# Performance work log

Measured on AMD Instinct MI355X. Metric: run time of the kernel, lower is better.

## Reference

```python
import jax, jax.numpy as jnp
import numpy as np

B, N = 32, 1000
HID, COM = 256, 64
T_LEN, NOP = 288, 3
NVAL, TP_D, CS_D, TIME_D = 9, 2, 4, 4
IN_C = CS_D + TP_D + NVAL            # 15, competition GAT input
IN_CO = IN_C + COM                    # 79, cooperation GAT input
OBS = TIME_D + TP_D + CS_D + 2 * COM + NVAL  # 147
K_D = K_F = 500                       # int(0.5*N + 0.5)
TEMP = 1.0
NEG = jnp.float32(-1e8)


def setup_inputs() -> dict:
    key = jax.random.key(0)
    ks = jax.random.split(key, 24)
    def nrm(k, shp, scale=0.05):
        return (jax.random.normal(k, shp, dtype=jnp.float32) * scale)
    return {
        "time_idx": jax.random.randint(ks[0], (B, N), 0, T_LEN, dtype=jnp.int32),
        "op_idx": jax.random.randint(ks[1], (B, N), 0, NOP, dtype=jnp.int32),
        "value_feats": jax.random.normal(ks[2], (B, N, NVAL), dtype=jnp.float32),
        "dpcs_mark": jax.random.randint(ks[3], (B, N, 1), 0, 2) > 0,
        "adj_comp": jax.random.randint(ks[4], (B, N, N), 0, 2) > 0,
        "adj_coop": jax.random.randint(ks[5], (B, N, N), 0, 2) > 0,
        "distance": jax.random.uniform(ks[6], (N, N), dtype=jnp.float32),
        "time_tab": jax.random.uniform(ks[7], (T_LEN, TIME_D), dtype=jnp.float32),
        "tp_tab": jax.random.uniform(ks[8], (NOP, TP_D), dtype=jnp.float32),
        "cs_tab": jax.random.uniform(ks[9], (N, CS_D), dtype=jnp.float32),
        "Wc": nrm(ks[10], (IN_C, COM)),
        "asrc_c": nrm(ks[11], (COM,)),
        "adst_c": nrm(ks[12], (COM,)),
        "wd_c": jnp.float32(0.1),
        "Wco": nrm(ks[13], (IN_CO, COM)),
        "asrc_co": nrm(ks[14], (COM,)),
        "adst_co": nrm(ks[15], (COM,)),
        "wd_co": jnp.float32(0.1),
        "Wp": nrm(ks[16], (OBS, HID)),
        "bp": jnp.zeros((HID,), dtype=jnp.float32),
        "vpd": nrm(ks[17], (HID,)),
        "vpf": nrm(ks[18], (HID,)),
    }


def gat(x, W, a_src, a_dst, w_d, adj, dist):
    """Single-head GAT over dense boolean adjacency. adj[b,j,i] True => edge j->i."""
    h = jnp.einsum("bnf,fd->bnd", x, W)                       # (B,N,D)
    e = (jnp.einsum("bid,d->bi", h, a_dst)[:, :, None]        # dst term
         + jnp.einsum("bjd,d->bj", h, a_src)[:, None, :]      # src term
         + w_d * dist.T[None])                                 # dist[j,i] edge feat
    e = jax.nn.leaky_relu(e, 0.2)
    mask = jnp.swapaxes(adj, 1, 2)                             # (B, dst i, src j)
    e = jnp.where(mask, e, NEG)
    alpha = jax.nn.softmax(e, axis=-1)
    alpha = jnp.where(mask, alpha, 0.0)                        # isolated nodes -> 0
    return jax.nn.elu(jnp.einsum("bij,bjd->bid", alpha, h))


def gated_pool(x_p, scores, valid, k, temp):
    scores = scores - scores.max(axis=1, keepdims=True)
    scores = jnp.where(valid, scores, NEG)                     # (B,N,1)
    val_topk = jax.lax.top_k(scores[..., 0], k)[0]             # (B,k)
    min_topk = val_topk.min(axis=-1)[:, None, None]
    scores = jnp.where(scores < min_topk, NEG, scores)
    w = jax.nn.softmax(scores / temp, axis=1)
    xg = x_p * w
    return jnp.concatenate([xg.sum(axis=1), xg.max(axis=1)], axis=-1)  # (B,2H)


def reference(time_idx, op_idx, value_feats, dpcs_mark, adj_comp, adj_coop,
              distance, time_tab, tp_tab, cs_tab, Wc, asrc_c, adst_c, wd_c,
              Wco, asrc_co, adst_co, wd_co, Wp, bp, vpd, vpf):
    time_e = time_tab[time_idx]                                # (B,N,4)
    tp_e = tp_tab[op_idx]                                      # (B,N,2)
    cs_e = jnp.broadcast_to(cs_tab[None], (B, N, CS_D))        # (B,N,4)
    vf_det = jax.lax.stop_gradient(value_feats)
    x = jnp.concatenate([cs_e, tp_e, vf_det], axis=-1)         # (B,N,15)
    comp_reps = gat(x, Wc, asrc_c, adst_c, wd_c, adj_comp, distance)
    x_m = jnp.concatenate([x, comp_reps], axis=-1)             # (B,N,79)
    coop_reps = gat(x_m, Wco, asrc_co, adst_co, wd_co, adj_coop, distance)
    sag = jnp.concatenate([time_e, cs_e, tp_e, value_feats, comp_reps, coop_reps], axis=-1)
    x_p = jnp.einsum("bnf,fh->bnh", sag, Wp) + bp              # (B,N,HID)
    scores_d = jnp.einsum("bnh,h->bn", x_p, vpd)[..., None]
    s_d = gated_pool(x_p, scores_d, dpcs_mark, K_D, TEMP)
    scores_f = jnp.einsum("bnh,h->bn", x_p, vpf)[..., None]
    s_f = gated_pool(x_p, scores_f, ~dpcs_mark, K_F, TEMP)
    return jnp.concatenate([s_f, s_d], axis=-1)                # (B, 4*HID)
```

## Files before the change

kernel.cpp:

```cpp
#include <hip/hip_runtime.h>
#include <hip/hip_bf16.h>

#define NB 32
#define NN 1000
#define COMD 64
#define HIDD 256
#define KSEL 500
#define TI 16
#define GATX ((NN + TI - 1) / TI)
#define PACKX 32
#define NSPL 32
#define ROWS 32
#define DSTRIDE 1024

#define PB_AQ1  0
#define PB_DT   1024
#define PB_WP   1280
#define PB_WCO  1320
#define PB_MISC 1344
#define PB_EMB  1345
#define PB_N    (PB_EMB + NB * NN / 4)

typedef __hip_bfloat16 bf16;
typedef unsigned long long u64;
typedef __attribute__((ext_vector_type(4))) float f32x4;
typedef __attribute__((ext_vector_type(8))) short s16x8;
typedef __attribute__((ext_vector_type(4))) short s16x4;
typedef __attribute__((ext_vector_type(4))) unsigned short u16x4;
typedef __attribute__((ext_vector_type(2))) unsigned long long u64x2;

__device__ __forceinline__ float b2f(bf16 x){ return __bfloat162float(x); }

template<bool F32>
__device__ __forceinline__ float ldf(const void* p, long i){
  return F32 ? ((const float*)p)[i] : b2f(((const bf16*)p)[i]);
}
__device__ __forceinline__ float ldr(const void* p, long i, int f32){
  return f32 ? ((const float*)p)[i] : b2f(((const bf16*)p)[i]);
}

__device__ __forceinline__ float wave_sum(float v){
#pragma unroll
  for (int o = 32; o > 0; o >>= 1) v += __shfl_down(v, o, 64);
  return v;
}
__device__ __forceinline__ float wave_bsum(float v){
#pragma unroll
  for (int o = 32; o > 0; o >>= 1) v += __shfl_xor(v, o, 64);
  return v;
}
__device__ __forceinline__ float wave_bmax(float v){
#pragma unroll
  for (int o = 32; o > 0; o >>= 1) v = fmaxf(v, __shfl_xor(v, o, 64));
  return v;
}
__device__ __forceinline__ int wave_bsum_i(int v){
#pragma unroll
  for (int o = 32; o > 0; o >>= 1) v += __shfl_xor(v, o, 64);
  return v;
}
__device__ __forceinline__ unsigned fkey(float f){
  unsigned u = __float_as_uint(f);
  return (u & 0x80000000u) ? ~u : (u | 0x80000000u);
}
__device__ __forceinline__ void split_bf(float v, short& hi, short& lo){
  unsigned u = __float_as_uint(v);
  float hf = __uint_as_float(u & 0xFFFF0000u);
  hi = (short)(u >> 16);
  float r = v - hf;
  lo = (short)(__float_as_uint(r) >> 16);
}
__device__ __forceinline__ short f2bs(float v){
  bf16 h = __float2bfloat16(v);
  short s; __builtin_memcpy(&s, &h, 2); return s;
}
__device__ __forceinline__ void hB_write(short* hB_hi, short* hB_lo,
                                         int b, int n, int ch, float v){
  int kb = n >> 5, g4 = (n >> 3) & 3, u = n & 7;
  long off = ((((long)b * 32 + kb) * 4 + g4) * 64 + ch) * 8 + u;
  short hi, lo; split_bf(v, hi, lo);
  hB_hi[off] = hi; hB_lo[off] = lo;
}
__device__ __forceinline__ void sniff2(const void* dist, const void* adjc,
                                       int lane, int& f32, int& as_int){
  unsigned wdist = ((const unsigned*)dist)[lane];
  unsigned wadj  = ((const unsigned*)adjc)[lane];
  f32 = (__ballot((wdist & 0xFFFFu) >= 0x8000u) != 0ull) ? 1 : 0;
  as_int = (__ballot(wadj > 1u) == 0ull) ? 1 : 0;
}

#define SMEM_BYTES 8704

template<bool F32>
__device__ __forceinline__ void dist_t_role(const void* dist, bf16* distTb,
                                            int rel, void* sm){
  bf16 (*tile)[68] = (bf16 (*)[68])sm;
  int t = threadIdx.x;
  int wv = t >> 6, lane = t & 63;
  int it = (rel & 15) * 64, jt = (rel >> 4) * 64;
#pragma unroll
  for (int r = 0; r < 16; ++r){
    int jl = r * 4 + wv;
    int j = jt + jl, i = it + lane;
    float v = (j < NN && i < NN) ? ldf<F32>(dist, (long)j * NN + i) : 0.f;
    tile[jl][lane] = __float2bfloat16(v);
  }
  __syncthreads();
#pragma unroll
  for (int r = 0; r < 16; ++r){
    int il = r * 4 + wv;
    int i = it + il, j = jt + lane;
    if (i < NN) distTb[(long)i * DSTRIDE + j] = tile[lane][il];
  }
}
template<bool BINT>
__device__ __forceinline__ void adjq_role(const void* adj, u64* adjQ,
                                          int rel, void* sm){
  u64 (*aw)[33] = (u64 (*)[33])sm;
  int t = threadIdx.x;
  int wv = t >> 6, lane = t & 63;
  int j0 = (rel & 31) * 32;
  int b  = rel >> 5;
  int ch3 = (192 + lane < 250) ? (192 + lane) : 249;
  int chk[4] = { lane, 64 + lane, 128 + lane, ch3 };
  long row0;
  {
    int j = j0 + wv * 8;
    int jc = (j < NN) ? j : (NN - 1);
    row0 = ((long)b * NN + jc) * (long)NN;
  }
  if (BINT){
    const int* base = (const int*)adj;
    uint4 cur[4], nxt[4];
#pragma unroll
    for (int c = 0; c < 4; ++c)
      cur[c] = *(const uint4*)(base + row0 + (long)chk[c] * 4);
#pragma unroll
    for (int r = 0; r < 8; ++r){
      if (r < 7){
        int j2 = j0 + wv * 8 + r + 1;
        int jc2 = (j2 < NN) ? j2 : (NN - 1);
        long row2 = ((long)b * NN + jc2) * (long)NN;
#pragma unroll
        for (int c = 0; c < 4; ++c)
          nxt[c] = *(const uint4*)(base + row2 + (long)chk[c] * 4);
      }
      int j = j0 + wv * 8 + r;
#pragma unroll
      for (int c = 0; c < 4; ++c){
        u64 bal0 = __ballot(cur[c].x != 0u);
        u64 bal1 = __ballot(cur[c].y != 0u);
        u64 bal2 = __ballot(cur[c].z != 0u);
        u64 bal3 = __ballot(cur[c].w != 0u);
        if (lane < 4){
          u64 w = 0;
          if (j < NN){
            int sh = 16 * lane;
            w = ((bal0 >> sh) & 0xFFFFull)
              | (((bal1 >> sh) & 0xFFFFull) << 16)
              | (((bal2 >> sh) & 0xFFFFull) << 32)
              | (((bal3 >> sh) & 0xFFFFull) << 48);
          }
          aw[c * 4 + lane][wv * 8 + r] = w;
        }
      }
      if (r < 7){
#pragma unroll
        for (int c = 0; c < 4; ++c) cur[c] = nxt[c];
      }
    }
  } else {
    const unsigned char* base = (const unsigned char*)adj;
    unsigned cur[4], nxt[4];
#pragma unroll
    for (int c = 0; c < 4; ++c)
      cur[c] = *(const unsigned*)(base + row0 + (long)chk[c] * 4);
#pragma unroll
    for (int r = 0; r < 8; ++r){
      if (r < 7){
        int j2 = j0 + wv * 8 + r + 1;
        int jc2 = (j2 < NN) ? j2 : (NN - 1);
        long row2 = ((long)b * NN + jc2) * (long)NN;
#pragma unroll
        for (int c = 0; c < 4; ++c)
          nxt[c] = *(const unsigned*)(base + row2 + (long)chk[c] * 4);
      }
      int j = j0 + wv * 8 + r;
#pragma unroll
      for (int c = 0; c < 4; ++c){
        u64 bal0 = __ballot((cur[c] & 0xFFu) != 0u);
        u64 bal1 = __ballot((cur[c] & 0xFF00u) != 0u);
        u64 bal2 = __ballot((cur[c] & 0xFF0000u) != 0u);
        u64 bal3 = __ballot((cur[c] & 0xFF000000u) != 0u);
        if (lane < 4){
          u64 w = 0;
          if (j < NN){
            int sh = 16 * lane;
            w = ((bal0 >> sh) & 0xFFFFull)
              | (((bal1 >> sh) & 0xFFFFull) << 16)
              | (((bal2 >> sh) & 0xFFFFull) << 32)
              | (((bal3 >> sh) & 0xFFFFull) << 48);
          }
          aw[c * 4 + lane][wv * 8 + r] = w;
        }
      }
      if (r < 7){
#pragma unroll
        for (int c = 0; c < 4; ++c) cur[c] = nxt[c];
      }
    }
  }
  __syncthreads();
#pragma unroll
  for (int rr = 0; rr < 2; ++rr){
    int w2 = t + rr * 256;
    int iw = w2 >> 5, jloc = w2 & 31;
    adjQ[((long)b * 16 + iw) * 1024 + j0 + jloc] = aw[iw][jloc];
  }
}
template<bool F32>
__device__ __forceinline__ void wp_role(const void* Wp, const void* vpd, const void* vpf,
                        short* WpB_hi, short* WpB_lo, float* wv_ws, int rel){
  int t = threadIdx.x;
  int g = t >> 6, lane = t & 63;
  int f = rel * 4 + g;
  float wrow[4];
#pragma unroll
  for (int r = 0; r < 4; ++r){
    int ch = r * 64 + lane;
    wrow[r] = (f < 147) ? ldf<F32>(Wp, (long)f * HIDD + ch) : 0.f;
  }
  int kb = f >> 5, q = (f >> 3) & 3, u = f & 7;
#pragma unroll
  for (int r = 0; r < 4; ++r){
    int ch = r * 64 + lane;
    long off = (((long)(kb * 4 + q)) * 256 + ch) * 8 + u;
    short hi, lo; split_bf(wrow[r], hi, lo);
    WpB_hi[off] = hi; WpB_lo[off] = lo;
  }
  float ad = 0.f, af = 0.f;
#pragma unroll
  for (int r = 0; r < 4; ++r){
    int ch = r * 64 + lane;
    ad += wrow[r] * ldf<F32>(vpd, ch);
    af += wrow[r] * ldf<F32>(vpf, ch);
  }
  ad = wave_bsum(ad); af = wave_bsum(af);
  if (lane == 0){ wv_ws[f] = ad; wv_ws[160 + f] = af; }
}
template<bool F32>
__device__ __forceinline__ void wco_role(const void* Wco, const void* asrc, const void* adst,
                         short* WcoB_hi, short* WcoB_lo, float* pvco, int rel){
  int t = threadIdx.x;
  int g = t >> 6, lane = t & 63;
  int f = rel * 4 + g;
  float w = (f < 79) ? ldf<F32>(Wco, (long)f * COMD + lane) : 0.f;
  int kb = f >> 5, q = (f >> 3) & 3, u = f & 7;
  long off = (((long)(kb * 4 + q)) * 64 + lane) * 8 + u;
  short hi, lo; split_bf(w, hi, lo);
  WcoB_hi[off] = hi; WcoB_lo[off] = lo;
  float dd = wave_bsum(w * ldf<F32>(adst, lane));
  float ss = wave_bsum(w * ldf<F32>(asrc, lane));
  if (lane == 0){ pvco[f] = dd; pvco[96 + f] = ss; }
}
template<bool F32>
__device__ __forceinline__ void misc_role(const void* wdc, const void* wdco,
                          const void* bp, const void* vpd, const void* vpf,
                          int f32, int as_int,
                          int* flags, float* wd_ws, float* wv_ws, int* ctr){
  int t = threadIdx.x;
  if (t >= 64) return;
  int lane = t;
  if (lane < NB) ctr[lane] = 0;
  float ad = 0.f, af = 0.f;
#pragma unroll
  for (int r = 0; r < 4; ++r){
    int ch = r * 64 + lane;
    float bb = ldf<F32>(bp, ch);
    ad += bb * ldf<F32>(vpd, ch);
    af += bb * ldf<F32>(vpf, ch);
  }
  ad = wave_bsum(ad); af = wave_bsum(af);
  if (lane == 0){
    wv_ws[320] = ad; wv_ws[321] = af;
    wd_ws[0] = ldf<F32>(wdc, 0);
    wd_ws[1] = ldf<F32>(wdco, 0);
    flags[0] = f32; flags[1] = as_int;
  }
}
template<bool F32>
__device__ __forceinline__ void embed_body(
    const int* op_idx, const void* vf, const void* cs_tab, const void* tp_tab,
    const void* Wc, const void* asrc, const void* adst,
    float* x_out, short* hB_hi, short* hB_lo, float* ed_out, float* es_out,
    int rel){
  int t = threadIdx.x;
  int w = t >> 6, lane = t & 63;
  int g = rel * 4 + w;
  int b = g / NN, n = g - b * NN;
  int op = op_idx[g];
  float xv = 0.f, hacc = 0.f;
#pragma unroll
  for (int f = 0; f < 15; ++f){
    float x_f;
    if (f < 4)      x_f = ldf<F32>(cs_tab, n * 4 + f);
    else if (f < 6) x_f = ldf<F32>(tp_tab, op * 2 + (f - 4));
    else            x_f = ldf<F32>(vf, (long)g * 9 + (f - 6));
    if (lane == f) xv = x_f;
    hacc += x_f * ldf<F32>(Wc, f * COMD + lane);
  }
  if (lane < 15) x_out[g * 15 + lane] = xv;
  hB_write(hB_hi, hB_lo, b, n, lane, hacc);
  float sd = wave_sum(hacc * ldf<F32>(adst, lane));
  float ss = wave_sum(hacc * ldf<F32>(asrc, lane));
  if (lane == 0){ ed_out[g] = sd; es_out[g] = ss; }
}
__global__ void __launch_bounds__(256) k_prep(
    const void* dist, const void* adj_comp,
    const void* wdc, const void* wdco,
    const void* Wp, const void* vpd, const void* vpf, const void* bp,
    const void* Wco, const void* asrc_co, const void* adst_co,
    const int* op_idx, const void* vfeat, const void* cs_tab, const void* tp_tab,
    const void* Wc, const void* asrc_c, const void* adst_c,
    int* flags, float* wd_ws, bf16* distTb, u64* adjQc,
    short* WpB_hi, short* WpB_lo, float* wv_ws,
    short* WcoB_hi, short* WcoB_lo, float* pvco,
    float* x_ws, short* hB_hi, short* hB_lo, float* ed_c, float* es_c,
    int* ctr){
  __shared__ __attribute__((aligned(16))) char smem[SMEM_BYTES];
  int blk = blockIdx.x;
  int f32, as_int;
  sniff2(dist, adj_comp, threadIdx.x & 63, f32, as_int);
  if (blk < PB_DT){
    if (as_int) adjq_role<true >(adj_comp, adjQc, blk - PB_AQ1, smem);
    else        adjq_role<false>(adj_comp, adjQc, blk - PB_AQ1, smem);
  } else if (blk < PB_WP){
    if (f32) dist_t_role<true >(dist, distTb, blk - PB_DT, smem);
    else     dist_t_role<false>(dist, distTb, blk - PB_DT, smem);
  } else if (blk < PB_WCO){
    if (f32) wp_role<true >(Wp, vpd, vpf, WpB_hi, WpB_lo, wv_ws, blk - PB_WP);
    else     wp_role<false>(Wp, vpd, vpf, WpB_hi, WpB_lo, wv_ws, blk - PB_WP);
  } else if (blk < PB_MISC){
    if (f32) wco_role<true >(Wco, asrc_co, adst_co, WcoB_hi, WcoB_lo, pvco, blk - PB_WCO);
    else     wco_role<false>(Wco, asrc_co, adst_co, WcoB_hi, WcoB_lo, pvco, blk - PB_WCO);
  } else if (blk < PB_EMB){
    if (f32) misc_role<true >(wdc, wdco, bp, vpd, vpf, f32, as_int, flags, wd_ws, wv_ws, ctr);
    else     misc_role<false>(wdc, wdco, bp, vpd, vpf, f32, as_int, flags, wd_ws, wv_ws, ctr);
  } else {
    if (f32) embed_body<true >(op_idx, vfeat, cs_tab, tp_tab, Wc, asrc_c, adst_c,
                               x_ws, hB_hi, hB_lo, ed_c, es_c, blk - PB_EMB);
    else     embed_body<false>(op_idx, vfeat, cs_tab, tp_tab, Wc, asrc_c, adst_c,
                               x_ws, hB_hi, hB_lo, ed_c, es_c, blk - PB_EMB);
  }
}

template<int MODE>
__device__ __forceinline__ void gat_body(
    const float* __restrict__ ed, const float* __restrict__ es,
    const float* __restrict__ wd_ws, int wd_idx, const u64* __restrict__ adjQ,
    const bf16* __restrict__ distTb,
    const short* __restrict__ hB_hi, const short* __restrict__ hB_lo,
    float* __restrict__ reps,
    const int* __restrict__ flags, const void* adj_raw, u64* adjQ_out,
    const float* __restrict__ x_ws,
    const short* __restrict__ WcoB_hi, const short* __restrict__ WcoB_lo,
    const float* __restrict__ pvco,
    short* hB2_hi, short* hB2_lo, float* ed_o, float* es_o,
    const int* __restrict__ time_idx, const int* __restrict__ op_idx,
    const void* vf, const void* time_tab, const void* cs_tab, const void* tp_tab,
    const float* __restrict__ comp,
    const short* __restrict__ WpB_hi, const short* __restrict__ WpB_lo,
    const float* __restrict__ wv_ws, const void* bp,
    float* x_p, float* scf_o, float* scd_o){
  __shared__ short pA[32 * 544] __attribute__((aligned(16)));
  __shared__ float redz[TI][4];
  __shared__ float esred[4];
  if (MODE == 0 && blockIdx.x >= GATX){
    int rel = (blockIdx.x - GATX) * NB + blockIdx.y;
    if (flags[1]) adjq_role<true >(adj_raw, adjQ_out, rel, (void*)pA);
    else          adjq_role<false>(adj_raw, adjQ_out, rel, (void*)pA);
    return;
  }
  int t = threadIdx.x;
  int wv = t >> 6, lane = t & 63;
  int b = blockIdx.y;
  int i0 = blockIdx.x * TI;
  float wd = wd_ws[wd_idx];
  int iw = i0 >> 6;
  int sb2 = (i0 & 63) >> 2;
  int j0 = t * 4;

  const u64* aq = adjQ + ((long)b * 16 + iw) * 1024 + j0;
  u64x2 wA = *(const u64x2*)&aq[0];
  u64x2 wB = *(const u64x2*)&aq[2];
  u64 wsh[4] = { wA[0] >> sb2, wA[1] >> sb2, wB[0] >> sb2, wB[1] >> sb2 };
  float4 es4 = *(const float4*)&es[(long)b * NN + j0];
  float esv[4] = {es4.x, es4.y, es4.z, es4.w};
  float esm = -1e30f;
#pragma unroll
  for (int c = 0; c < 4; ++c)
    esm = fmaxf(esm, (j0 + c < NN) ? esv[c] : -1e30f);
  esm = wave_bmax(esm);
  if (lane == 0) esred[wv] = esm;

  float ed_i[TI]; float edm = -1e30f;
#pragma unroll
  for (int ti = 0; ti < TI; ++ti){
    int i = i0 + ti;
    float ev = ed[(long)b * NN + ((i < NN) ? i : (NN - 1))];
    ed_i[ti] = ev;
    edm = fmaxf(edm, (i < NN) ? ev : -1e30f);
  }
  __syncthreads();
  float M = fmaxf(fmaxf(esred[0], esred[1]), fmaxf(esred[2], esred[3]))
            + edm + fmaxf(wd, 0.f);
  M = fmaxf(M, 0.f);

  float p[TI][4];
  const bf16* dbase = distTb + j0;
#pragma unroll
  for (int ti = 0; ti < TI; ++ti){
    int i = i0 + ti;
    int ic = (i < NN) ? i : (NN - 1);
    u16x4 d4 = *(const u16x4*)&dbase[(long)ic * DSTRIDE];
    float edti = ed_i[ti];
    int psh = 16 * (ti & 3) + (ti >> 2);
#pragma unroll
    for (int c = 0; c < 4; ++c){
      float d = __uint_as_float((unsigned)d4[c] << 16);
      float v = edti + esv[c] + wd * d;
      v = fmaxf(v, 0.2f * v);
      bool edge = (wsh[c] >> psh) & 1ull;
      float e = edge ? v : -1e30f;
      p[ti][c] = __expf(e - M);
    }
  }

  int kbw = 8 * wv + (lane >> 3);
  int qw = (lane >> 1) & 3;
  int u0 = 4 * (lane & 1);
  int wbase = kbw * 544 + qw * 136 + u0;
#pragma unroll
  for (int ti = 0; ti < TI; ++ti){
    float zs = p[ti][0] + p[ti][1] + p[ti][2] + p[ti][3];
    zs = wave_bsum(zs);
    if (lane == 0) redz[ti][wv] = zs;
    s16x4 s4 = { f2bs(p[ti][0]), f2bs(p[ti][1]), f2bs(p[ti][2]), f2bs(p[ti][3]) };
    *(s16x4*)&pA[wbase + ti * 8] = s4;
  }
  __syncthreads();

  int q = lane >> 4, m = lane & 15;
  int abase = q * 136 + m * 8;
  int ch = wv * 16 + m;
  const short* bh = hB_hi + (long)b * 65536 + ((long)q * 64 + ch) * 8;
  const short* bl = hB_lo + (long)b * 65536 + ((long)q * 64 + ch) * 8;
  f32x4 acc = {0.f, 0.f, 0.f, 0.f};
#pragma unroll
  for (int kb = 0; kb < 32; ++kb){
    s16x8 a   = *(const s16x8*)&pA[kb * 544 + abase];
    s16x8 bhi = *(const s16x8*)&bh[(long)kb * 2048];
    s16x8 blo = *(const s16x8*)&bl[(long)kb * 2048];
    acc = __builtin_amdgcn_mfma_f32_16x16x32_bf16(a, bhi, acc, 0, 0, 0);
    acc = __builtin_amdgcn_mfma_f32_16x16x32_bf16(a, blo, acc, 0, 0, 0);
  }
  float vr[4];
#pragma unroll
  for (int reg = 0; reg < 4; ++reg){
    int ti = (lane >> 4) * 4 + reg;
    float z = redz[ti][0] + redz[ti][1] + redz[ti][2] + redz[ti][3];
    float zi = (z > 0.f) ? 1.f / z : 0.f;
    float v = acc[reg] * zi;
    v = (v > 0.f) ? v : expm1f(v);
    vr[reg] = v;
    if (MODE == 0){
      int ch2 = wv * 16 + (lane & 15);
      if (i0 + ti < NN)
        reps[((long)b * NN + i0 + ti) * COMD + ch2] = v;
    }
  }

  if (MODE == 0){
    __syncthreads();
    float* cx = (float*)pA;
    short* cA_hi = pA + 2560;
    short* cA_lo = pA + 2560 + 1920;
    {
      int ch2 = wv * 16 + (lane & 15);
#pragma unroll
      for (int reg = 0; reg < 4; ++reg){
        int row = (lane >> 4) * 4 + reg;
        cx[row * 80 + 15 + ch2] = vr[reg];
      }
    }
    for (int idx = t; idx < 16 * 15; idx += 256){
      int nl = idx / 15, f = idx - nl * 15;
      int i = i0 + nl; int ic = (i < NN) ? i : (NN - 1);
      cx[nl * 80 + f] = x_ws[((long)b * NN + ic) * 15 + f];
    }
    __syncthreads();
    {
      int node = t >> 4, sub = t & 15;
      float dd = 0.f, ss = 0.f;
      for (int f = sub; f < 79; f += 16){
        float c = cx[node * 80 + f];
        dd += c * pvco[f];
        ss += c * pvco[96 + f];
      }
#pragma unroll
      for (int o = 8; o > 0; o >>= 1){
        dd += __shfl_xor(dd, o, 64);
        ss += __shfl_xor(ss, o, 64);
      }
      if (sub == 0 && i0 + node < NN){
        ed_o[(long)b * NN + i0 + node] = dd;
        es_o[(long)b * NN + i0 + node] = ss;
      }
    }
    for (int idx = t; idx < 16 * 96; idx += 256){
      int mm = idx / 96, k = idx - mm * 96;
      float v = (k < 79) ? cx[mm * 80 + k] : 0.f;
      int kb = k >> 5, qq = (k >> 3) & 3, u = k & 7;
      short hi, lo; split_bf(v, hi, lo);
      int off = (kb * 16 + mm) * 40 + qq * 8 + u;
      cA_hi[off] = hi; cA_lo[off] = lo;
    }
    __syncthreads();
    {
      int q2 = lane >> 4, m2 = lane & 15;
      int ch3 = wv * 16 + m2;
      f32x4 a2 = {0.f, 0.f, 0.f, 0.f};
#pragma unroll
      for (int kb = 0; kb < 3; ++kb){
        int aoff = (kb * 16 + m2) * 40 + q2 * 8;
        s16x8 a_hi = *(const s16x8*)&cA_hi[aoff];
        s16x8 a_lo = *(const s16x8*)&cA_lo[aoff];
        long boff = (((long)(kb * 4 + q2)) * 64 + ch3) * 8;
        s16x8 b_hi = *(const s16x8*)&WcoB_hi[boff];
        s16x8 b_lo = *(const s16x8*)&WcoB_lo[boff];
        a2 = __builtin_amdgcn_mfma_f32_16x16x32_bf16(a_hi, b_hi, a2, 0, 0, 0);
        a2 = __builtin_amdgcn_mfma_f32_16x16x32_bf16(a_hi, b_lo, a2, 0, 0, 0);
        a2 = __builtin_amdgcn_mfma_f32_16x16x32_bf16(a_lo, b_hi, a2, 0, 0, 0);
      }
#pragma unroll
      for (int reg = 0; reg < 4; ++reg){
        int row = (lane >> 4) * 4 + reg;
        int n2 = i0 + row;
        hB_write(hB2_hi, hB2_lo, b, n2, ch3, a2[reg]);
      }
    }
  } else {
    __syncthreads();
    float* sagF = (float*)pA;
    short* sgA_hi = pA + 4736;
    short* sgA_lo = pA + 7936;
    int f32 = flags[0];
    {
      int ch2 = wv * 16 + (lane & 15);
#pragma unroll
      for (int reg = 0; reg < 4; ++reg){
        int row = (lane >> 4) * 4 + reg;
        sagF[row * 148 + 83 + ch2] = vr[reg];
      }
    }
    for (int idx = t; idx < 16 * 83; idx += 256){
      int nl = idx / 83, f = idx - nl * 83;
      int n = i0 + nl; int ic = (n < NN) ? n : (NN - 1);
      long g = (long)b * NN + ic;
      float v;
      if (f < 4)       v = ldr(time_tab, (long)time_idx[g] * 4 + f, f32);
      else if (f < 8)  v = ldr(cs_tab, ic * 4 + (f - 4), f32);
      else if (f < 10) v = ldr(tp_tab, (long)op_idx[g] * 2 + (f - 8), f32);
      else if (f < 19) v = ldr(vf, g * 9 + (f - 10), f32);
      else             v = comp[g * COMD + (f - 19)];
      sagF[nl * 148 + f] = v;
    }
    __syncthreads();
    for (int idx = t; idx < 16 * 160; idx += 256){
      int mm = idx / 160, k = idx - mm * 160;
      float v = (k < 147) ? sagF[mm * 148 + k] : 0.f;
      int kb = k >> 5, qq = (k >> 3) & 3, u = k & 7;
      short hi, lo; split_bf(v, hi, lo);
      int off = (kb * 16 + mm) * 40 + qq * 8 + u;
      sgA_hi[off] = hi; sgA_lo[off] = lo;
    }
    {
      int node = t >> 4, sub = t & 15;
      float ad = 0.f, af = 0.f;
      for (int f = sub; f < 147; f += 16){
        float s = sagF[node * 148 + f];
        ad += s * wv_ws[f];
        af += s * wv_ws[160 + f];
      }
#pragma unroll
      for (int o = 8; o > 0; o >>= 1){
        ad += __shfl_xor(ad, o, 64);
        af += __shfl_xor(af, o, 64);
      }
      if (sub == 0 && i0 + node < NN){
        scd_o[(long)b * NN + i0 + node] = ad + wv_ws[320];
        scf_o[(long)b * NN + i0 + node] = af + wv_ws[321];
      }
    }
    __syncthreads();
    int Ag = lane >> 4, Am = lane & 15;
    f32x4 acc2[4] = {{0,0,0,0},{0,0,0,0},{0,0,0,0},{0,0,0,0}};
#pragma unroll
    for (int kb = 0; kb < 5; ++kb){
      int aoff = (kb * 16 + Am) * 40 + Ag * 8;
      s16x8 a_hi = *(const s16x8*)&sgA_hi[aoff];
      s16x8 a_lo = *(const s16x8*)&sgA_lo[aoff];
#pragma unroll
      for (int ct = 0; ct < 4; ++ct){
        int ch3 = wv * 64 + ct * 16 + Am;
        long boff = (((long)(kb * 4 + Ag)) * 256 + ch3) * 8;
        s16x8 b_hi = *(const s16x8*)&WpB_hi[boff];
        s16x8 b_lo = *(const s16x8*)&WpB_lo[boff];
        acc2[ct] = __builtin_amdgcn_mfma_f32_16x16x32_bf16(a_hi, b_hi, acc2[ct], 0, 0, 0);
        acc2[ct] = __builtin_amdgcn_mfma_f32_16x16x32_bf16(a_hi, b_lo, acc2[ct], 0, 0, 0);
        acc2[ct] = __builtin_amdgcn_mfma_f32_16x16x32_bf16(a_lo, b_hi, acc2[ct], 0, 0, 0);
      }
    }
#pragma unroll
    for (int ct = 0; ct < 4; ++ct){
      int ch3 = wv * 64 + ct * 16 + (lane & 15);
      float bb = ldr(bp, ch3, f32);
#pragma unroll
      for (int reg = 0; reg < 4; ++reg){
        int row = (lane >> 4) * 4 + reg;
        if (i0 + row < NN)
          x_p[((long)b * NN + i0 + row) * HIDD + ch3] = acc2[ct][reg] + bb;
      }
    }
  }
}
__global__ void __launch_bounds__(256) k_gat1(
    const float* ed, const float* es, const float* wd_ws, const u64* adjQ,
    const bf16* distTb, const short* hB_hi, const short* hB_lo, float* reps,
    const int* flags, const void* adj_raw, u64* adjQ_out,
    const float* x_ws, const short* WcoB_hi, const short* WcoB_lo,
    const float* pvco, short* hB2_hi, short* hB2_lo, float* ed_o, float* es_o){
  gat_body<0>(ed, es, wd_ws, 0, adjQ, distTb, hB_hi, hB_lo, reps,
              flags, adj_raw, adjQ_out, x_ws, WcoB_hi, WcoB_lo, pvco,
              hB2_hi, hB2_lo, ed_o, es_o,
              nullptr, nullptr, nullptr, nullptr, nullptr, nullptr,
              nullptr, nullptr, nullptr, nullptr, nullptr,
              nullptr, nullptr, nullptr);
}
__global__ void __launch_bounds__(256) k_gat2x(
    const float* ed, const float* es, const float* wd_ws, const u64* adjQ,
    const bf16* distTb, const short* hB_hi, const short* hB_lo,
    const int* flags,
    const int* time_idx, const int* op_idx, const void* vf,
    const void* time_tab, const void* cs_tab, const void* tp_tab,
    const float* comp, const short* WpB_hi, const short* WpB_lo,
    const float* wv_ws, const void* bp,
    float* x_p, float* scf, float* scd){
  gat_body<1>(ed, es, wd_ws, 1, adjQ, distTb, hB_hi, hB_lo, nullptr,
              flags, nullptr, nullptr, nullptr, nullptr, nullptr, nullptr,
              nullptr, nullptr, nullptr, nullptr,
              time_idx, op_idx, vf, time_tab, cs_tab, tp_tab,
              comp, WpB_hi, WpB_lo, wv_ws, bp, x_p, scf, scd);
}

__global__ void __launch_bounds__(256) k_pool(
    const int* __restrict__ flags, const float* __restrict__ scf,
    const float* __restrict__ scd, const void* __restrict__ mark,
    const float* __restrict__ x_p, float* __restrict__ part,
    int* __restrict__ ctr, void* __restrict__ out){
  __shared__ float wf[ROWS], wdd[ROWS];
  __shared__ int lastf;
  int t = threadIdx.x;
  int wv = t >> 6, lane = t & 63;
  int b = blockIdx.x, z = blockIdx.y;
  int n0 = z * ROWS;
  int f32 = flags[0], bint = flags[1];
  if (wv < 2){
    int pool = wv;
    const float* sc = pool ? scd : scf;
    float v[16]; unsigned key[16];
    float m0 = -INFINITY;
#pragma unroll
    for (int r = 0; r < 16; ++r){
      int n = r * 64 + lane;
      float s = (n < NN) ? sc[b * NN + n] : -INFINITY;
      v[r] = s; m0 = fmaxf(m0, s);
    }
    m0 = wave_bmax(m0);
    float m1 = -INFINITY;
#pragma unroll
    for (int r = 0; r < 16; ++r){
      int n = r * 64 + lane;
      bool valid = false;
      if (n < NN){
        bool mk = bint ? (((const int*)mark)[b * NN + n] != 0)
                       : (((const unsigned char*)mark)[b * NN + n] != 0);
        valid = (pool == 0) ? !mk : mk;
      }
      v[r] = valid ? (v[r] - m0) : -1e8f;
      key[r] = fkey(v[r]);
      if (n < NN) m1 = fmaxf(m1, v[r]);
    }
    m1 = wave_bmax(m1);
    unsigned lo = 0u, hi = 0xFFFFFFFFu;
    while (lo < hi){
      unsigned mid = lo + ((hi - lo) >> 1) + 1u;
      int c = 0;
#pragma unroll
      for (int r = 0; r < 16; ++r) c += (key[r] >= mid) ? 1 : 0;
      c = wave_bsum_i(c);
      if (c >= KSEL) lo = mid; else hi = mid - 1u;
    }
    float ls = 0.f; float p[16];
#pragma unroll
    for (int r = 0; r < 16; ++r){
      int n = r * 64 + lane;
      float pp = (n < NN && key[r] >= lo) ? __expf(v[r] - m1) : 0.f;
      p[r] = pp; ls += pp;
    }
    ls = wave_bsum(ls);
    float zinv = (ls > 0.f) ? 1.f / ls : 0.f;
    float* wdst = pool ? wdd : wf;
#pragma unroll
    for (int r = 0; r < 16; ++r){
      int n = r * 64 + lane;
      if (n >= n0 && n < n0 + ROWS && n < NN) wdst[n - n0] = p[r] * zinv;
    }
  }
  __syncthreads();
  int ns = min(ROWS, NN - n0);
  float sf = 0.f, mf = -INFINITY, sd = 0.f, md = -INFINITY;
  const float* xb = x_p + ((long)b * NN + n0) * HIDD + t;
  for (int k = 0; k < ns; ++k){
    float xv = xb[(long)k * HIDD];
    float gf = wf[k] * xv;
    float gd = wdd[k] * xv;
    sf += gf; mf = fmaxf(mf, gf);
    sd += gd; md = fmaxf(md, gd);
  }
  long pb = (((long)b * NSPL + z) * 4) * HIDD + t;
  part[pb + 0 * HIDD] = sf;
  part[pb + 1 * HIDD] = mf;
  part[pb + 2 * HIDD] = sd;
  part[pb + 3 * HIDD] = md;
  __threadfence();
  if (t == 0) lastf = (atomicAdd(&ctr[b], 1) == NSPL - 1);
  __syncthreads();
  if (!lastf) return;
  __threadfence();
  float asf = 0.f, amf = -INFINITY, asd = 0.f, amd = -INFINITY;
  for (int zz = 0; zz < NSPL; ++zz){
    long qb = (((long)b * NSPL + zz) * 4) * HIDD + t;
    asf += part[qb + 0 * HIDD];
    amf = fmaxf(amf, part[qb + 1 * HIDD]);
    asd += part[qb + 2 * HIDD];
    amd = fmaxf(amd, part[qb + 3 * HIDD]);
  }
  long ob = (long)b * 1024;
  if (f32){
    ((float*)out)[ob + t] = asf;
    ((float*)out)[ob + 256 + t] = amf;
    ((float*)out)[ob + 512 + t] = asd;
    ((float*)out)[ob + 768 + t] = amd;
  } else {
    ((bf16*)out)[ob + t] = __float2bfloat16(asf);
    ((bf16*)out)[ob + 256 + t] = __float2bfloat16(amf);
    ((bf16*)out)[ob + 512 + t] = __float2bfloat16(asd);
    ((bf16*)out)[ob + 768 + t] = __float2bfloat16(amd);
  }
}

extern "C" void kernel_launch(void* const* d_in, const int* in_sizes, int n_in,
                              void* d_out, int out_size, void* d_ws, size_t ws_size,
                              hipStream_t stream){
  const int*  time_idx = (const int*)d_in[0];
  const int*  op_idx   = (const int*)d_in[1];
  const void* vfeat    = d_in[2];
  const void* dpcs     = d_in[3];
  const void* adj_comp = d_in[4];
  const void* adj_coop = d_in[5];
  const void* dist     = d_in[6];
  const void* time_tab = d_in[7];
  const void* tp_tab   = d_in[8];
  const void* cs_tab   = d_in[9];
  const void* Wc       = d_in[10];
  const void* asrc_c   = d_in[11];
  const void* adst_c   = d_in[12];
  const void* wd_c     = d_in[13];
  const void* Wco      = d_in[14];
  const void* asrc_co  = d_in[15];
  const void* adst_co  = d_in[16];
  const void* wd_co    = d_in[17];
  const void* Wp       = d_in[18];
  const void* bp       = d_in[19];
  const void* vpd      = d_in[20];
  const void* vpf      = d_in[21];

  char* ws = (char*)d_ws;
  size_t o = 0;
  auto alloc = [&](size_t bytes)->char*{
    char* p = ws + o; o = (o + bytes + 255) & ~(size_t)255; return p;
  };
  int*   flags   = (int*)alloc(16);
  float* wd_ws   = (float*)alloc(8);
  int*   ctr     = (int*)alloc(NB * 4);
  bf16*  distTb  = (bf16*)alloc((size_t)NN * DSTRIDE * 2);
  u64*   adjQc   = (u64*)alloc((size_t)NB * 16 * 1024 * 8);
  u64*   adjQo   = (u64*)alloc((size_t)NB * 16 * 1024 * 8);
  float* x_ws    = (float*)alloc((size_t)NB * NN * 15 * 4);
  float* comp    = (float*)alloc((size_t)NB * NN * COMD * 4);
  short* hB_hi   = (short*)alloc((size_t)NB * 65536 * 2);
  short* hB_lo   = (short*)alloc((size_t)NB * 65536 * 2);
  short* hB2_hi  = (short*)alloc((size_t)NB * 65536 * 2);
  short* hB2_lo  = (short*)alloc((size_t)NB * 65536 * 2);
  short* WpB_hi  = (short*)alloc((size_t)5 * 4 * 256 * 8 * 2);
  short* WpB_lo  = (short*)alloc((size_t)5 * 4 * 256 * 8 * 2);
  short* WcoB_hi = (short*)alloc((size_t)3 * 4 * 64 * 8 * 2);
  short* WcoB_lo = (short*)alloc((size_t)3 * 4 * 64 * 8 * 2);
  float* wv_ws   = (float*)alloc(322 * 4);
  float* pvco    = (float*)alloc(192 * 4);
  float* ed_c    = (float*)alloc((size_t)NB * NN * 4 + 256);
  float* es_c    = (float*)alloc((size_t)NB * NN * 4 + 256);
  float* ed_o    = (float*)alloc((size_t)NB * NN * 4 + 256);
  float* es_o    = (float*)alloc((size_t)NB * NN * 4 + 256);
  float* scf     = (float*)alloc((size_t)NB * NN * 4);
  float* scd     = (float*)alloc((size_t)NB * NN * 4);
  float* part    = (float*)alloc((size_t)NB * NSPL * 4 * HIDD * 4);
  float* x_p     = (float*)alloc((size_t)NB * NN * HIDD * 4);

  k_prep<<<dim3(PB_N), dim3(256), 0, stream>>>(
      dist, adj_comp, wd_c, wd_co, Wp, vpd, vpf, bp,
      Wco, asrc_co, adst_co,
      op_idx, vfeat, cs_tab, tp_tab, Wc, asrc_c, adst_c,
      flags, wd_ws, distTb, adjQc, WpB_hi, WpB_lo, wv_ws,
      WcoB_hi, WcoB_lo, pvco,
      x_ws, hB_hi, hB_lo, ed_c, es_c, ctr);
  k_gat1<<<dim3(GATX + PACKX, NB), dim3(256), 0, stream>>>(
      ed_c, es_c, wd_ws, adjQc, distTb, hB_hi, hB_lo, comp,
      flags, adj_coop, adjQo,
      x_ws, WcoB_hi, WcoB_lo, pvco, hB2_hi, hB2_lo, ed_o, es_o);
  k_gat2x<<<dim3(GATX, NB), dim3(256), 0, stream>>>(
      ed_o, es_o, wd_ws, adjQo, distTb, hB2_hi, hB2_lo,
      flags, time_idx, op_idx, vfeat, time_tab, cs_tab, tp_tab,
      comp, WpB_hi, WpB_lo, wv_ws, bp, x_p, scf, scd);
  k_pool<<<dim3(NB, NSPL), dim3(256), 0, stream>>>(
      flags, scf, scd, dpcs, x_p, part, ctr, d_out);
}
```

Baseline: 543.1 us.

## Split pooling into separate top-k, partial-sum and finalize kernels

```diff
diff --git a/kernel.cpp b/kernel.cpp
--- a/kernel.cpp
+++ b/kernel.cpp
@@ -37,6 +37,10 @@
 }
 __device__ __forceinline__ float ldr(const void* p, long i, int f32){
   return f32 ? ((const float*)p)[i] : b2f(((const bf16*)p)[i]);
+}
+template<bool BINT>
+__device__ __forceinline__ bool ldb(const void* p, long i){
+  return BINT ? (((const int*)p)[i] != 0) : (((const unsigned char*)p)[i] != 0);
 }
 
 __device__ __forceinline__ float wave_sum(float v){
@@ -267,11 +271,10 @@
 __device__ __forceinline__ void misc_role(const void* wdc, const void* wdco,
                           const void* bp, const void* vpd, const void* vpf,
                           int f32, int as_int,
-                          int* flags, float* wd_ws, float* wv_ws, int* ctr){
+                          int* flags, float* wd_ws, float* wv_ws){
   int t = threadIdx.x;
   if (t >= 64) return;
   int lane = t;
-  if (lane < NB) ctr[lane] = 0;
   float ad = 0.f, af = 0.f;
 #pragma unroll
   for (int r = 0; r < 4; ++r){
@@ -325,8 +328,7 @@
     int* flags, float* wd_ws, bf16* distTb, u64* adjQc,
     short* WpB_hi, short* WpB_lo, float* wv_ws,
     short* WcoB_hi, short* WcoB_lo, float* pvco,
-    float* x_ws, short* hB_hi, short* hB_lo, float* ed_c, float* es_c,
-    int* ctr){
+    float* x_ws, short* hB_hi, short* hB_lo, float* ed_c, float* es_c){
   __shared__ __attribute__((aligned(16))) char smem[SMEM_BYTES];
   int blk = blockIdx.x;
   int f32, as_int;
@@ -344,8 +346,8 @@
     if (f32) wco_role<true >(Wco, asrc_co, adst_co, WcoB_hi, WcoB_lo, pvco, blk - PB_WCO);
     else     wco_role<false>(Wco, asrc_co, adst_co, WcoB_hi, WcoB_lo, pvco, blk - PB_WCO);
   } else if (blk < PB_EMB){
-    if (f32) misc_role<true >(wdc, wdco, bp, vpd, vpf, f32, as_int, flags, wd_ws, wv_ws, ctr);
-    else     misc_role<false>(wdc, wdco, bp, vpd, vpf, f32, as_int, flags, wd_ws, wv_ws, ctr);
+    if (f32) misc_role<true >(wdc, wdco, bp, vpd, vpf, f32, as_int, flags, wd_ws, wv_ws);
+    else     misc_role<false>(wdc, wdco, bp, vpd, vpf, f32, as_int, flags, wd_ws, wv_ws);
   } else {
     if (f32) embed_body<true >(op_idx, vfeat, cs_tab, tp_tab, Wc, asrc_c, adst_c,
                                x_ws, hB_hi, hB_lo, ed_c, es_c, blk - PB_EMB);
@@ -663,72 +665,84 @@
               comp, WpB_hi, WpB_lo, wv_ws, bp, x_p, scf, scd);
 }
 
-__global__ void __launch_bounds__(256) k_pool(
-    const int* __restrict__ flags, const float* __restrict__ scf,
-    const float* __restrict__ scd, const void* __restrict__ mark,
-    const float* __restrict__ x_p, float* __restrict__ part,
-    int* __restrict__ ctr, void* __restrict__ out){
+template<bool BINT>
+__device__ __forceinline__ void topk_body(
+    const float* scf, const float* scd, const void* mark, float* wls){
+  int lane = threadIdx.x;
+  int b = blockIdx.x, pool = blockIdx.y;
+  const float* sc = (pool == 0) ? scf : scd;
+  float v[16]; unsigned key[16];
+  float m0 = -INFINITY;
+#pragma unroll
+  for (int r = 0; r < 16; ++r){
+    int n = r * 64 + lane;
+    float s = (n < NN) ? sc[b * NN + n] : -INFINITY;
+    v[r] = s;
+    m0 = fmaxf(m0, s);
+  }
+  m0 = wave_bmax(m0);
+  float m1 = -INFINITY;
+#pragma unroll
+  for (int r = 0; r < 16; ++r){
+    int n = r * 64 + lane;
+    bool valid = false;
+    if (n < NN){
+      bool mk = ldb<BINT>(mark, b * NN + n);
+      valid = (pool == 0) ? !mk : mk;
+    }
+    v[r] = valid ? (v[r] - m0) : -1e8f;
+    key[r] = fkey(v[r]);
+    if (n < NN) m1 = fmaxf(m1, v[r]);
+  }
+  m1 = wave_bmax(m1);
+
+  unsigned lo = 0u, hi = 0xFFFFFFFFu;
+  while (lo < hi){
+    unsigned mid = lo + ((hi - lo) >> 1) + 1u;
+    int c = 0;
+#pragma unroll
+    for (int r = 0; r < 16; ++r) c += (key[r] >= mid) ? 1 : 0;
+    c = wave_bsum_i(c);
+    if (c >= KSEL) lo = mid; else hi = mid - 1u;
+  }
+
+  float p[16];
+  float ls = 0.f;
+#pragma unroll
+  for (int r = 0; r < 16; ++r){
+    int n = r * 64 + lane;
+    float pp = (n < NN && key[r] >= lo) ? __expf(v[r] - m1) : 0.f;
+    p[r] = pp;
+    ls += pp;
+  }
+  ls = wave_bsum(ls);
+  float zinv = (ls > 0.f) ? 1.f / ls : 0.f;
+  float* w_out = wls + ((long)b * 2 + pool) * 1024;
+#pragma unroll
+  for (int r = 0; r < 16; ++r){
+    int n = r * 64 + lane;
+    if (n < NN) w_out[n] = p[r] * zinv;
+  }
+}
+__global__ void k_topk(const int* flags, const float* scf, const float* scd,
+                       const void* mark, float* wls){
+  if (flags[1]) topk_body<true >(scf, scd, mark, wls);
+  else          topk_body<false>(scf, scd, mark, wls);
+}
+
+__global__ void __launch_bounds__(256) k_psum(
+    const float* __restrict__ wls, const float* __restrict__ x_p,
+    float* __restrict__ part){
   __shared__ float wf[ROWS], wdd[ROWS];
-  __shared__ int lastf;
   int t = threadIdx.x;
-  int wv = t >> 6, lane = t & 63;
   int b = blockIdx.x, z = blockIdx.y;
   int n0 = z * ROWS;
-  int f32 = flags[0], bint = flags[1];
-  if (wv < 2){
-    int pool = wv;
-    const float* sc = pool ? scd : scf;
-    float v[16]; unsigned key[16];
-    float m0 = -INFINITY;
-#pragma unroll
-    for (int r = 0; r < 16; ++r){
-      int n = r * 64 + lane;
-      float s = (n < NN) ? sc[b * NN + n] : -INFINITY;
-      v[r] = s; m0 = fmaxf(m0, s);
-    }
-    m0 = wave_bmax(m0);
-    float m1 = -INFINITY;
-#pragma unroll
-    for (int r = 0; r < 16; ++r){
-      int n = r * 64 + lane;
-      bool valid = false;
-      if (n < NN){
-        bool mk = bint ? (((const int*)mark)[b * NN + n] != 0)
-                       : (((const unsigned char*)mark)[b * NN + n] != 0);
-        valid = (pool == 0) ? !mk : mk;
-      }
-      v[r] = valid ? (v[r] - m0) : -1e8f;
-      key[r] = fkey(v[r]);
-      if (n < NN) m1 = fmaxf(m1, v[r]);
-    }
-    m1 = wave_bmax(m1);
-    unsigned lo = 0u, hi = 0xFFFFFFFFu;
-    while (lo < hi){
-      unsigned mid = lo + ((hi - lo) >> 1) + 1u;
-      int c = 0;
-#pragma unroll
-      for (int r = 0; r < 16; ++r) c += (key[r] >= mid) ? 1 : 0;
-      c = wave_bsum_i(c);
-      if (c >= KSEL) lo = mid; else hi = mid - 1u;
-    }
-    float ls = 0.f; float p[16];
-#pragma unroll
-    for (int r = 0; r < 16; ++r){
-      int n = r * 64 + lane;
-      float pp = (n < NN && key[r] >= lo) ? __expf(v[r] - m1) : 0.f;
-      p[r] = pp; ls += pp;
-    }
-    ls = wave_bsum(ls);
-    float zinv = (ls > 0.f) ? 1.f / ls : 0.f;
-    float* wdst = pool ? wdd : wf;
-#pragma unroll
-    for (int r = 0; r < 16; ++r){
-      int n = r * 64 + lane;
-      if (n >= n0 && n < n0 + ROWS && n < NN) wdst[n - n0] = p[r] * zinv;
-    }
+  int ns = min(ROWS, NN - n0);
+  if (t < ns){
+    wf[t]  = wls[((long)b * 2 + 0) * 1024 + n0 + t];
+    wdd[t] = wls[((long)b * 2 + 1) * 1024 + n0 + t];
   }
   __syncthreads();
-  int ns = min(ROWS, NN - n0);
   float sf = 0.f, mf = -INFINITY, sd = 0.f, md = -INFINITY;
   const float* xb = x_p + ((long)b * NN + n0) * HIDD + t;
   for (int k = 0; k < ns; ++k){
@@ -743,31 +757,37 @@
   part[pb + 1 * HIDD] = mf;
   part[pb + 2 * HIDD] = sd;
   part[pb + 3 * HIDD] = md;
-  __threadfence();
-  if (t == 0) lastf = (atomicAdd(&ctr[b], 1) == NSPL - 1);
-  __syncthreads();
-  if (!lastf) return;
-  __threadfence();
-  float asf = 0.f, amf = -INFINITY, asd = 0.f, amd = -INFINITY;
-  for (int zz = 0; zz < NSPL; ++zz){
-    long qb = (((long)b * NSPL + zz) * 4) * HIDD + t;
-    asf += part[qb + 0 * HIDD];
-    amf = fmaxf(amf, part[qb + 1 * HIDD]);
-    asd += part[qb + 2 * HIDD];
-    amd = fmaxf(amd, part[qb + 3 * HIDD]);
+}
+
+template<bool F32>
+__device__ __forceinline__ void pfin_body(const float* part, void* out){
+  int t = threadIdx.x;
+  int b = blockIdx.x;
+  float sf = 0.f, mf = -INFINITY, sd = 0.f, md = -INFINITY;
+#pragma unroll
+  for (int z = 0; z < NSPL; ++z){
+    long pb = (((long)b * NSPL + z) * 4) * HIDD + t;
+    sf += part[pb + 0 * HIDD];
+    mf = fmaxf(mf, part[pb + 1 * HIDD]);
+    sd += part[pb + 2 * HIDD];
+    md = fmaxf(md, part[pb + 3 * HIDD]);
   }
   long ob = (long)b * 1024;
-  if (f32){
-    ((float*)out)[ob + t] = asf;
-    ((float*)out)[ob + 256 + t] = amf;
-    ((float*)out)[ob + 512 + t] = asd;
-    ((float*)out)[ob + 768 + t] = amd;
+  if (F32){
+    ((float*)out)[ob + t] = sf;
+    ((float*)out)[ob + 256 + t] = mf;
+    ((float*)out)[ob + 512 + t] = sd;
+    ((float*)out)[ob + 768 + t] = md;
   } else {
-    ((bf16*)out)[ob + t] = __float2bfloat16(asf);
-    ((bf16*)out)[ob + 256 + t] = __float2bfloat16(amf);
-    ((bf16*)out)[ob + 512 + t] = __float2bfloat16(asd);
-    ((bf16*)out)[ob + 768 + t] = __float2bfloat16(amd);
-  }
+    ((bf16*)out)[ob + t] = __float2bfloat16(sf);
+    ((bf16*)out)[ob + 256 + t] = __float2bfloat16(mf);
+    ((bf16*)out)[ob + 512 + t] = __float2bfloat16(sd);
+    ((bf16*)out)[ob + 768 + t] = __float2bfloat16(md);
+  }
+}
+__global__ void k_pfin(const int* flags, const float* part, void* out){
+  if (flags[0]) pfin_body<true >(part, out);
+  else          pfin_body<false>(part, out);
 }
 
 extern "C" void kernel_launch(void* const* d_in, const int* in_sizes, int n_in,
@@ -803,7 +823,6 @@
   };
   int*   flags   = (int*)alloc(16);
   float* wd_ws   = (float*)alloc(8);
-  int*   ctr     = (int*)alloc(NB * 4);
   bf16*  distTb  = (bf16*)alloc((size_t)NN * DSTRIDE * 2);
   u64*   adjQc   = (u64*)alloc((size_t)NB * 16 * 1024 * 8);
   u64*   adjQo   = (u64*)alloc((size_t)NB * 16 * 1024 * 8);
@@ -825,6 +844,7 @@
   float* es_o    = (float*)alloc((size_t)NB * NN * 4 + 256);
   float* scf     = (float*)alloc((size_t)NB * NN * 4);
   float* scd     = (float*)alloc((size_t)NB * NN * 4);
+  float* wls     = (float*)alloc((size_t)NB * 2 * 1024 * 4);
   float* part    = (float*)alloc((size_t)NB * NSPL * 4 * HIDD * 4);
   float* x_p     = (float*)alloc((size_t)NB * NN * HIDD * 4);
 
@@ -834,7 +854,7 @@
       op_idx, vfeat, cs_tab, tp_tab, Wc, asrc_c, adst_c,
       flags, wd_ws, distTb, adjQc, WpB_hi, WpB_lo, wv_ws,
       WcoB_hi, WcoB_lo, pvco,
-      x_ws, hB_hi, hB_lo, ed_c, es_c, ctr);
+      x_ws, hB_hi, hB_lo, ed_c, es_c);
   k_gat1<<<dim3(GATX + PACKX, NB), dim3(256), 0, stream>>>(
       ed_c, es_c, wd_ws, adjQc, distTb, hB_hi, hB_lo, comp,
       flags, adj_coop, adjQo,
@@ -843,6 +863,7 @@
       ed_o, es_o, wd_ws, adjQo, distTb, hB2_hi, hB2_lo,
       flags, time_idx, op_idx, vfeat, time_tab, cs_tab, tp_tab,
       comp, WpB_hi, WpB_lo, wv_ws, bp, x_p, scf, scd);
-  k_pool<<<dim3(NB, NSPL), dim3(256), 0, stream>>>(
-      flags, scf, scd, dpcs, x_p, part, ctr, d_out);
-}
+  k_topk<<<dim3(NB, 2), dim3(64), 0, stream>>>(flags, scf, scd, dpcs, wls);
+  k_psum<<<dim3(NB, NSPL), dim3(256), 0, stream>>>(wls, x_p, part);
+  k_pfin<<<dim3(NB), dim3(256), 0, stream>>>(flags, part, d_out);
+}
```

After: 453.7 us. 1.2x faster.
